# Kernel optimization log

Hardware: AMD Instinct MI355X
Metric: run time of the kernel (lower is better)

Reference implementation:

```python
import jax, jax.numpy as jnp
import numpy as np

B, C, H, W = 16, 512, 32, 32
HW = H * W  # == input_features == output_features for shapes to be consistent


def setup_inputs() -> dict:
    key = jax.random.key(0)
    k1, k2, k3 = jax.random.split(key, 3)
    node1 = jax.random.normal(k1, (B, C, H, W), dtype=jnp.float32)
    node2 = jax.random.normal(k2, (B, C, H, W), dtype=jnp.float32)
    # nn.Linear(input_features, output_features, bias=False).weight: [out, in]
    W_c = jax.random.normal(k3, (HW, HW), dtype=jnp.float32) * (1.0 / np.sqrt(HW))
    return {"node1": node1, "node2": node2, "W_c": W_c}


def reference(node1, node2, W_c):
    b, c, h, w = node1.shape
    hw = h * w
    n1 = node1.reshape(b, c, hw)  # [B, C, HW]
    n2 = node2.reshape(b, c, hw)  # [B, C, HW]
    # x = W_c(n1): Linear applies y = x @ W^T  -> [B, C, HW_out]
    x = jnp.einsum('bch,oh->bco', n1, W_c)
    # e = bmm(x.permute(0,2,1), n2): [B, HW_out, C] @ [B, C, HW] -> [B, HW_out, HW]
    e = jnp.einsum('bco,bch->boh', x, n2)
    a = jax.nn.softmax(e, axis=-1)  # softmax over last dim (HW of node2)
    # m = bmm(n2, a): [B, C, HW] @ [B, HW, HW] -> [B, C, HW]
    m = jnp.einsum('bck,bkj->bcj', n2, a)
    return m
```

## Files before the change

kernel.cpp:

```cpp
#include <hip/hip_runtime.h>
#include <math.h>


typedef _Float16 f16;
typedef _Float16 f16x8 __attribute__((ext_vector_type(8)));
typedef _Float16 f16x4 __attribute__((ext_vector_type(4)));
typedef float f32x4 __attribute__((ext_vector_type(4)));

#define L2E 1.442695040888963f

#define WG_BARRIER() asm volatile("s_waitcnt lgkmcnt(0)\ns_barrier" ::: "memory")

__device__ __forceinline__ f16x8 cvt8(f32x4 lo, f32x4 hi) {
    f16x8 o;
#pragma unroll
    for (int i = 0; i < 4; ++i) { o[i] = (f16)lo[i]; o[4 + i] = (f16)hi[i]; }
    return o;
}

__device__ __forceinline__ f16x8 expb(f16x8 b, f32x4 cl, f32x4 ch) {
    f16x8 t;
#pragma unroll
    for (int i = 0; i < 4; ++i) t[i] = (f16)exp2f(fmaf((float)b[i], L2E, -cl[i]));
#pragma unroll
    for (int i = 0; i < 4; ++i) t[4 + i] = (f16)exp2f(fmaf((float)b[4 + i], L2E, -ch[i]));
    return t;
}

__global__ __launch_bounds__(256) void prep(const float* __restrict__ Wc,
                                            const float* __restrict__ n2,
                                            f16* __restrict__ Wf,
                                            f16* __restrict__ n2t) {
    const int bid = blockIdx.x, tid = threadIdx.x;
    if (bid < 512) {
        const size_t i = ((size_t)bid * 256 + tid) * 8;
        f32x4 a = *(const f32x4*)(Wc + i);
        f32x4 b = *(const f32x4*)(Wc + i + 4);
        *(f16x8*)(Wf + i) = cvt8(a, b);
        return;
    }
    const int id = bid - 512;
    const int b = id >> 7;
    const int ry = (id & 127) >> 4;
    const int cx = id & 15;
    const float* S = n2 + (size_t)b * 512 * 1024;
    f16* Dt = n2t + (size_t)b * 1024 * 512;
    __shared__ f16 Ts[64 * 72];
    const int r0 = ry * 64, c0 = cx * 64;
    const int rr = tid >> 3, cc8 = (tid & 7) * 8;
#pragma unroll
    for (int h = 0; h < 2; ++h) {
        const int row = r0 + rr + 32 * h;
        const float* s = S + (size_t)row * 1024 + c0 + cc8;
        f32x4 a = *(const f32x4*)s, bq = *(const f32x4*)(s + 4);
        *(f16x8*)&Ts[(rr + 32 * h) * 72 + cc8] = cvt8(a, bq);
    }
    __syncthreads();
    const int j = tid >> 2, k16 = (tid & 3) * 16;
    f16* d = Dt + (size_t)(c0 + j) * 512 + r0 + k16;
    f16x8 o0, o1;
#pragma unroll
    for (int i = 0; i < 8; ++i) {
        o0[i] = Ts[(k16 + i) * 72 + j];
        o1[i] = Ts[(k16 + 8 + i) * 72 + j];
    }
    *(f16x8*)d = o0;
    *(f16x8*)(d + 8) = o1;
}

__global__ __launch_bounds__(256) void stats_combine(const float* __restrict__ Pm,
                                                     const float* __restrict__ Ps,
                                                     float* __restrict__ Sc) {
    const int g = blockIdx.x * 256 + threadIdx.x;
    const int b = g >> 10, o = g & 1023;
    const int mt = o >> 8, ml = o & 255;
    const float* pm = Pm + ((size_t)(b * 4 + mt) * 8) * 256 + ml;
    const float* ps = Ps + ((size_t)(b * 4 + mt) * 8) * 256 + ml;
    float M = -3.0e38f;
#pragma unroll
    for (int p = 0; p < 8; ++p) M = fmaxf(M, pm[p * 256]);
    float S = 0.f;
#pragma unroll
    for (int p = 0; p < 8; ++p) S += ps[p * 256] * exp2f(pm[p * 256] - M);
    Sc[g] = M + __log2f(S);
}

template <int NS>
__device__ __forceinline__ void gemm_core(const char* gA0, const char* gA1,
                                          const char* gB, char* SM, int sOff,
                                          int wm, int wn, int col, int swz16,
                                          f32x4 (&acc)[4][4]) {
    f16x8 a00 = *(const f16x8*)gA0, a01 = *(const f16x8*)gA1;
    f16x8 b0 = *(const f16x8*)gB;
    {
        char* dA = SM + sOff;
        *(f16x8*)dA = a00;
        *(f16x8*)(dA + 8192) = a01;
        *(f16x8*)(SM + 32768 + sOff) = b0;
    }
    f16x8 a10 = *(const f16x8*)(gA0 + 64), a11 = *(const f16x8*)(gA1 + 64);
    f16x8 b1 = *(const f16x8*)(gB + 64);
    a00 = *(const f16x8*)(gA0 + 128); a01 = *(const f16x8*)(gA1 + 128);
    b0 = *(const f16x8*)(gB + 128);
    WG_BARRIER();
#pragma unroll
    for (int kb = 0; kb < NS; ++kb) {
        const char* Ac = SM + (kb & 1) * 16384;
        const char* Bc = SM + 32768 + (kb & 1) * 8192;
        f16x8 fa[4], fb[4];
#pragma unroll
        for (int u = 0; u < 4; ++u)
            fa[u] = *(const f16x8*)(Ac + (wm + u * 16 + col) * 64 + swz16);
#pragma unroll
        for (int v = 0; v < 4; ++v)
            fb[v] = *(const f16x8*)(Bc + (wn + v * 16 + col) * 64 + swz16);
#pragma unroll
        for (int u = 0; u < 4; ++u)
#pragma unroll
            for (int v = 0; v < 4; ++v)
                acc[u][v] = __builtin_amdgcn_mfma_f32_16x16x32_f16(fa[u], fb[v],
                                                                   acc[u][v], 0, 0, 0);
        if (kb + 1 < NS) {
            char* dA = SM + ((kb + 1) & 1) * 16384 + sOff;
            char* dB = SM + 32768 + ((kb + 1) & 1) * 8192 + sOff;
            if ((kb & 1) == 0) {
                *(f16x8*)dA = a10;
                *(f16x8*)(dA + 8192) = a11;
                *(f16x8*)dB = b1;
                if (kb + 3 < NS) {
                    a10 = *(const f16x8*)(gA0 + (size_t)(kb + 3) * 64);
                    a11 = *(const f16x8*)(gA1 + (size_t)(kb + 3) * 64);
                    b1 = *(const f16x8*)(gB + (size_t)(kb + 3) * 64);
                }
            } else {
                *(f16x8*)dA = a00;
                *(f16x8*)(dA + 8192) = a01;
                *(f16x8*)dB = b0;
                if (kb + 3 < NS) {
                    a00 = *(const f16x8*)(gA0 + (size_t)(kb + 3) * 64);
                    a01 = *(const f16x8*)(gA1 + (size_t)(kb + 3) * 64);
                    b0 = *(const f16x8*)(gB + (size_t)(kb + 3) * 64);
                }
            }
            WG_BARRIER();
        }
    }
}

template <int NS, bool EXPB>
__device__ __forceinline__ void gemm_core_a32(const char* gA0, const char* gA1,
                                              const char* gB, const float* gSp,
                                              char* SM, int sOff, int wm, int wn,
                                              int col, int swz16, f32x4 (&acc)[4][4]) {
    f32x4 c00, c01, c10, c11;
    f32x4 a00l = *(const f32x4*)gA0, a00h = *(const f32x4*)(gA0 + 16);
    f32x4 a01l = *(const f32x4*)gA1, a01h = *(const f32x4*)(gA1 + 16);
    f16x8 b0 = *(const f16x8*)gB;
    if (EXPB) { c00 = *(const f32x4*)gSp; c01 = *(const f32x4*)(gSp + 4); }
    {
        char* dA = SM + sOff;
        *(f16x8*)dA = cvt8(a00l, a00h);
        *(f16x8*)(dA + 8192) = cvt8(a01l, a01h);
        char* dB = SM + 32768 + sOff;
        *(f16x8*)dB = EXPB ? expb(b0, c00, c01) : b0;
    }
    f32x4 a10l = *(const f32x4*)(gA0 + 128), a10h = *(const f32x4*)(gA0 + 144);
    f32x4 a11l = *(const f32x4*)(gA1 + 128), a11h = *(const f32x4*)(gA1 + 144);
    f16x8 b1 = *(const f16x8*)(gB + 64);
    if (EXPB) { c10 = *(const f32x4*)(gSp + 32); c11 = *(const f32x4*)(gSp + 36); }
    a00l = *(const f32x4*)(gA0 + 256); a00h = *(const f32x4*)(gA0 + 272);
    a01l = *(const f32x4*)(gA1 + 256); a01h = *(const f32x4*)(gA1 + 272);
    b0 = *(const f16x8*)(gB + 128);
    if (EXPB) { c00 = *(const f32x4*)(gSp + 64); c01 = *(const f32x4*)(gSp + 68); }
    WG_BARRIER();
#pragma unroll
    for (int kb = 0; kb < NS; ++kb) {
        const char* Ac = SM + (kb & 1) * 16384;
        const char* Bc = SM + 32768 + (kb & 1) * 8192;
        f16x8 fa[4], fb[4];
#pragma unroll
        for (int u = 0; u < 4; ++u)
            fa[u] = *(const f16x8*)(Ac + (wm + u * 16 + col) * 64 + swz16);
#pragma unroll
        for (int v = 0; v < 4; ++v)
            fb[v] = *(const f16x8*)(Bc + (wn + v * 16 + col) * 64 + swz16);
#pragma unroll
        for (int u = 0; u < 4; ++u)
#pragma unroll
            for (int v = 0; v < 4; ++v)
                acc[u][v] = __builtin_amdgcn_mfma_f32_16x16x32_f16(fa[u], fb[v],
                                                                   acc[u][v], 0, 0, 0);
        if (kb + 1 < NS) {
            char* dA = SM + ((kb + 1) & 1) * 16384 + sOff;
            char* dB = SM + 32768 + ((kb + 1) & 1) * 8192 + sOff;
            if ((kb & 1) == 0) {
                *(f16x8*)dA = cvt8(a10l, a10h);
                *(f16x8*)(dA + 8192) = cvt8(a11l, a11h);
                *(f16x8*)dB = EXPB ? expb(b1, c10, c11) : b1;
                if (kb + 3 < NS) {
                    a10l = *(const f32x4*)(gA0 + (size_t)(kb + 3) * 128);
                    a10h = *(const f32x4*)(gA0 + (size_t)(kb + 3) * 128 + 16);
                    a11l = *(const f32x4*)(gA1 + (size_t)(kb + 3) * 128);
                    a11h = *(const f32x4*)(gA1 + (size_t)(kb + 3) * 128 + 16);
                    b1 = *(const f16x8*)(gB + (size_t)(kb + 3) * 64);
                    if (EXPB) {
                        c10 = *(const f32x4*)(gSp + (size_t)(kb + 3) * 32);
                        c11 = *(const f32x4*)(gSp + (size_t)(kb + 3) * 32 + 4);
                    }
                }
            } else {
                *(f16x8*)dA = cvt8(a00l, a00h);
                *(f16x8*)(dA + 8192) = cvt8(a01l, a01h);
                *(f16x8*)dB = EXPB ? expb(b0, c00, c01) : b0;
                if (kb + 3 < NS) {
                    a00l = *(const f32x4*)(gA0 + (size_t)(kb + 3) * 128);
                    a00h = *(const f32x4*)(gA0 + (size_t)(kb + 3) * 128 + 16);
                    a01l = *(const f32x4*)(gA1 + (size_t)(kb + 3) * 128);
                    a01h = *(const f32x4*)(gA1 + (size_t)(kb + 3) * 128 + 16);
                    b0 = *(const f16x8*)(gB + (size_t)(kb + 3) * 64);
                    if (EXPB) {
                        c00 = *(const f32x4*)(gSp + (size_t)(kb + 3) * 32);
                        c01 = *(const f32x4*)(gSp + (size_t)(kb + 3) * 32 + 4);
                    }
                }
            }
            WG_BARRIER();
        }
    }
}

__device__ __forceinline__ void epilogue_tr(f32x4 (&acc)[4][4], char* SM, f16* dst0,
                                            int dstRow, int m0, int n0, int tid) {
    const int lane = tid & 63, wave = tid >> 6;
    const int col = lane & 15, quad = lane >> 4;
    const int wn = (wave >> 2) * 64;
    const int mh_w = (wave >> 1) & 1;
    const int wm_loc = (wave & 1) * 64;
    const int j = tid >> 2, seg = (tid & 3) * 32;
    WG_BARRIER();
    f16* Tt = (f16*)SM;
#pragma unroll
    for (int mh = 0; mh < 2; ++mh) {
        if (mh_w == mh) {
#pragma unroll
            for (int u = 0; u < 4; ++u)
#pragma unroll
                for (int v = 0; v < 4; ++v) {
                    f16x4 p;
#pragma unroll
                    for (int r = 0; r < 4; ++r) p[r] = (f16)acc[u][v][r];
                    *(f16x4*)&Tt[(wn + v * 16 + col) * 136 + wm_loc + u * 16 + quad * 4] = p;
                }
        }
        WG_BARRIER();
        f16* dst = dst0 + (size_t)(n0 + j) * dstRow + m0 + mh * 128 + seg;
#pragma unroll
        for (int c8 = 0; c8 < 32; c8 += 8)
            *(f16x8*)(dst + c8) = *(const f16x8*)&Tt[j * 136 + seg + c8];
        if (mh == 0) WG_BARRIER();
    }
}

__global__ __launch_bounds__(512) void gemm1_nt_xt(const float* __restrict__ A,
                                                   const f16* __restrict__ Bw,
                                                   f16* __restrict__ Xt) {
    const int K = 1024;
    const int id = blockIdx.x;
    const int xcd = id & 7, loc = id >> 3;
    const int b = xcd * 2 + (loc >> 4);
    const int m0 = ((loc >> 3) & 1) * 256;
    const int n0 = (loc & 7) * 128;
    A += (size_t)b * 512 * K;
    Xt += (size_t)b * 1024 * 512;
    __shared__ __attribute__((aligned(16))) char SM[49152];
    const int tid = threadIdx.x, lane = tid & 63, wave = tid >> 6;
    const int col = lane & 15, quad = lane >> 4;
    const int wm = (wave & 3) * 64, wn = (wave >> 2) * 64;
    const int srow = tid >> 2, sslot = tid & 3;
    const int sOff = srow * 64 + ((sslot ^ ((srow >> 1) & 3)) * 16);
    const int swz16 = (quad ^ ((col >> 1) & 3)) * 16;
    const char* gA0 = (const char*)A + (size_t)(m0 + srow) * K * 4 + sslot * 32;
    const char* gA1 = gA0 + (size_t)128 * K * 4;
    const char* gB = (const char*)Bw + (size_t)(n0 + srow) * K * 2 + sslot * 16;
    f32x4 acc[4][4] = {};
    gemm_core_a32<32, false>(gA0, gA1, gB, nullptr, SM, sOff, wm, wn, col, swz16, acc);
    epilogue_tr(acc, SM, Xt, 512, m0, n0, tid);
}

__global__ __launch_bounds__(512) void gemm2_nt_et(const f16* __restrict__ A,
                                                   const f16* __restrict__ B,
                                                   f16* __restrict__ Et,
                                                   float* __restrict__ Pm,
                                                   float* __restrict__ Ps) {
    const int K = 512;
    const int id = blockIdx.x;
    const int xcd = id & 7, loc = id >> 3;
    const int b = xcd * 2 + (loc >> 5);
    const int m0 = ((loc >> 3) & 3) * 256;
    const int n0 = (loc & 7) * 128;
    A += (size_t)b * 1024 * K;
    B += (size_t)b * 1024 * K;
    Et += (size_t)b * 1024 * 1024;
    __shared__ __attribute__((aligned(16))) char SM[49152];
    const int tid = threadIdx.x, lane = tid & 63, wave = tid >> 6;
    const int col = lane & 15, quad = lane >> 4;
    const int wm = (wave & 3) * 64, wn = (wave >> 2) * 64;
    const int srow = tid >> 2, sslot = tid & 3;
    const int sOff = srow * 64 + ((sslot ^ ((srow >> 1) & 3)) * 16);
    const int swz16 = (quad ^ ((col >> 1) & 3)) * 16;
    const char* gA0 = (const char*)A + (size_t)(m0 + srow) * K * 2 + sslot * 16;
    const char* gA1 = gA0 + (size_t)128 * K * 2;
    const char* gB = (const char*)B + (size_t)(n0 + srow) * K * 2 + sslot * 16;
    f32x4 acc[4][4] = {};
    gemm_core<16>(gA0, gA1, gB, SM, sOff, wm, wn, col, swz16, acc);

    {
        const int wn_e = (wave >> 2) * 64;
        const int mh_w = (wave >> 1) & 1;
        const int wm_loc = (wave & 1) * 64;
        const int j = tid >> 2, seg = (tid & 3) * 32;
        const int scol = tid >> 2, srq = tid & 3;
        WG_BARRIER();
        f16* Tt = (f16*)SM;
#pragma unroll
        for (int mh = 0; mh < 2; ++mh) {
            if (mh_w == mh) {
#pragma unroll
                for (int u = 0; u < 4; ++u)
#pragma unroll
                    for (int v = 0; v < 4; ++v) {
                        f16x4 p;
#pragma unroll
                        for (int r = 0; r < 4; ++r) p[r] = (f16)acc[u][v][r];
                        *(f16x4*)&Tt[(wn_e + v * 16 + col) * 136 + wm_loc + u * 16 + quad * 4] = p;
                    }
            }
            WG_BARRIER();
            f16* dst = Et + (size_t)(n0 + j) * 1024 + m0 + mh * 128 + seg;
#pragma unroll
            for (int c8 = 0; c8 < 32; c8 += 8)
                *(f16x8*)(dst + c8) = *(const f16x8*)&Tt[j * 136 + seg + c8];
            float mx = -3.0e38f;
#pragma unroll
            for (int n = 0; n < 32; ++n) {
                const int row = srq * 32 + ((n + scol) & 31);
                mx = fmaxf(mx, (float)Tt[row * 136 + scol]);
            }
            const float mxl = mx * L2E;
            float s = 0.f;
#pragma unroll
            for (int n = 0; n < 32; ++n) {
                const int row = srq * 32 + ((n + scol) & 31);
                s += exp2f(fmaf((float)Tt[row * 136 + scol], L2E, -mxl));
            }
            float pmv = mxl, psv = s;
#pragma unroll
            for (int d = 1; d < 4; d <<= 1) {
                float om = __shfl_xor(pmv, d, 64);
                float os = __shfl_xor(psv, d, 64);
                float nm = fmaxf(pmv, om);
                psv = psv * exp2f(pmv - nm) + os * exp2f(om - nm);
                pmv = nm;
            }
            if (srq == 0) {
                const int part = (b * 4 + (m0 >> 8)) * 8 + (n0 >> 7);
                const int ml = mh * 128 + scol;
                Pm[(size_t)part * 256 + ml] = pmv;
                Ps[(size_t)part * 256 + ml] = psv;
            }
            if (mh == 0) WG_BARRIER();
        }
    }
}

__global__ __launch_bounds__(512) void gemm3_nt_out(const float* __restrict__ A,
                                                    const f16* __restrict__ Et,
                                                    const float* __restrict__ Sc,
                                                    float* __restrict__ C) {
    const int K = 1024;
    const int id = blockIdx.x;
    const int xcd = id & 7, loc = id >> 3;
    const int b = xcd * 2 + (loc >> 4);
    const int m0 = ((loc >> 3) & 1) * 256;
    const int n0 = (loc & 7) * 128;
    A += (size_t)b * 512 * K;
    Et += (size_t)b * 1024 * K;
    Sc += (size_t)b * 1024;
    C += (size_t)b * 512 * 1024;
    __shared__ __attribute__((aligned(16))) char SM[49152];
    const int tid = threadIdx.x, lane = tid & 63, wave = tid >> 6;
    const int col = lane & 15, quad = lane >> 4;
    const int wm = (wave & 3) * 64, wn = (wave >> 2) * 64;
    const int srow = tid >> 2, sslot = tid & 3;
    const int sOff = srow * 64 + ((sslot ^ ((srow >> 1) & 3)) * 16);
    const int swz16 = (quad ^ ((col >> 1) & 3)) * 16;
    const char* gA0 = (const char*)A + (size_t)(m0 + srow) * K * 4 + sslot * 32;
    const char* gA1 = gA0 + (size_t)128 * K * 4;
    const char* gB = (const char*)Et + (size_t)(n0 + srow) * K * 2 + sslot * 16;
    const float* gSp = Sc + sslot * 8;
    f32x4 acc[4][4] = {};
    gemm_core_a32<32, true>(gA0, gA1, gB, gSp, SM, sOff, wm, wn, col, swz16, acc);

#pragma unroll
    for (int u = 0; u < 4; ++u)
#pragma unroll
        for (int v = 0; v < 4; ++v)
#pragma unroll
            for (int r = 0; r < 4; ++r)
                C[(size_t)(m0 + wm + u * 16 + quad * 4 + r) * 1024 + n0 + wn + v * 16 + col] =
                    acc[u][v][r];
}

extern "C" void kernel_launch(void* const* d_in, const int* in_sizes, int n_in,
                              void* d_out, int out_size, void* d_ws, size_t ws_size,
                              hipStream_t stream) {
    const float* n1 = (const float*)d_in[0];
    const float* n2 = (const float*)d_in[1];
    const float* Wc = (const float*)d_in[2];
    float* out = (float*)d_out;
    char* ws = (char*)d_ws;

    f16* n2t = (f16*)(ws);
    f16* Xt  = (f16*)(ws + (16u << 20));
    f16* Wf  = (f16*)(ws + (32u << 20));
    f16* Et  = (f16*)(ws + (32u << 20));
    float* Pm = (float*)(ws + (64u << 20));
    float* Ps = (float*)(ws + (65u << 20));
    float* Sc = (float*)(ws + (66u << 20));

    prep<<<2560, dim3(256), 0, stream>>>(Wc, n2, Wf, n2t);
    gemm1_nt_xt<<<256, dim3(512), 0, stream>>>(n1, Wf, Xt);
    gemm2_nt_et<<<512, dim3(512), 0, stream>>>(Xt, n2t, Et, Pm, Ps);
    stats_combine<<<64, dim3(256), 0, stream>>>(Pm, Ps, Sc);
    gemm3_nt_out<<<256, dim3(512), 0, stream>>>(n2, Et, Sc, out);
}
```

Before: 204.1 us.

## Use direct global-to-LDS loads in GEMMs and pre-convert node1 to fp16

Replaces the register-staged double-buffered loads in gemm1 and gemm2 with global_load_lds DMA transfers into a swizzled LDS layout, synchronised through vmcnt waits and barriers. To make gemm1 fit this path, node1 is now converted to fp16 in the prep kernel instead of inside gemm1. The aim is to free registers and VALU work spent staging tiles and to overlap global loads with MFMA. The cost is an extra fp16 copy of node1 written to and read back from global memory, plus an added barrier per k-step.

Result: no change. 200.4 us (-1.8%).

```diff
diff --git a/kernel.cpp b/kernel.cpp
--- a/kernel.cpp
+++ b/kernel.cpp
@@ -11,6 +11,11 @@
 
 #define WG_BARRIER() asm volatile("s_waitcnt lgkmcnt(0)\ns_barrier" ::: "memory")
 
+#define DMA16(g, l)                                                             \
+    __builtin_amdgcn_global_load_lds(                                           \
+        (const __attribute__((address_space(1))) void*)(g),                     \
+        (__attribute__((address_space(3))) void*)(l), 16, 0, 0)
+
 __device__ __forceinline__ f16x8 cvt8(f32x4 lo, f32x4 hi) {
     f16x8 o;
 #pragma unroll
@@ -27,19 +32,22 @@
     return t;
 }
 
-__global__ __launch_bounds__(256) void prep(const float* __restrict__ Wc,
+__global__ __launch_bounds__(256) void prep(const float* __restrict__ n1,
+                                            const float* __restrict__ Wc,
                                             const float* __restrict__ n2,
-                                            f16* __restrict__ Wf,
+                                            f16* __restrict__ n1f, f16* __restrict__ Wf,
                                             f16* __restrict__ n2t) {
     const int bid = blockIdx.x, tid = threadIdx.x;
-    if (bid < 512) {
-        const size_t i = ((size_t)bid * 256 + tid) * 8;
-        f32x4 a = *(const f32x4*)(Wc + i);
-        f32x4 b = *(const f32x4*)(Wc + i + 4);
-        *(f16x8*)(Wf + i) = cvt8(a, b);
+    if (bid < 4608) {
+        const float* s = (bid < 4096) ? n1 : Wc;
+        f16* d = (bid < 4096) ? n1f : Wf;
+        const size_t i = ((size_t)(bid < 4096 ? bid : bid - 4096) * 256 + tid) * 8;
+        f32x4 a = *(const f32x4*)(s + i);
+        f32x4 b = *(const f32x4*)(s + i + 4);
+        *(f16x8*)(d + i) = cvt8(a, b);
         return;
     }
-    const int id = bid - 512;
+    const int id = bid - 4608;
     const int b = id >> 7;
     const int ry = (id & 127) >> 4;
     const int cx = id & 15;
@@ -86,25 +94,18 @@
 }
 
 template <int NS>
-__device__ __forceinline__ void gemm_core(const char* gA0, const char* gA1,
-                                          const char* gB, char* SM, int sOff,
-                                          int wm, int wn, int col, int swz16,
-                                          f32x4 (&acc)[4][4]) {
-    f16x8 a00 = *(const f16x8*)gA0, a01 = *(const f16x8*)gA1;
-    f16x8 b0 = *(const f16x8*)gB;
-    {
-        char* dA = SM + sOff;
-        *(f16x8*)dA = a00;
-        *(f16x8*)(dA + 8192) = a01;
-        *(f16x8*)(SM + 32768 + sOff) = b0;
-    }
-    f16x8 a10 = *(const f16x8*)(gA0 + 64), a11 = *(const f16x8*)(gA1 + 64);
-    f16x8 b1 = *(const f16x8*)(gB + 64);
-    a00 = *(const f16x8*)(gA0 + 128); a01 = *(const f16x8*)(gA1 + 128);
-    b0 = *(const f16x8*)(gB + 128);
-    WG_BARRIER();
+__device__ __forceinline__ void gemm_dmac(const char* sA0, const char* sA1,
+                                          const char* sB, char* dA, char* dB,
+                                          char* SM, int wm, int wn, int col,
+                                          int swz16, f32x4 (&acc)[4][4]) {
+    DMA16(sA0, dA); DMA16(sA1, dA + 8192); DMA16(sB, dB);
+    DMA16(sA0 + 64, dA + 16384); DMA16(sA1 + 64, dA + 24576); DMA16(sB + 64, dB + 8192);
 #pragma unroll
     for (int kb = 0; kb < NS; ++kb) {
+        if (kb + 1 < NS) asm volatile("s_waitcnt vmcnt(3)" ::: "memory");
+        else             asm volatile("s_waitcnt vmcnt(0)" ::: "memory");
+        __builtin_amdgcn_s_barrier();
+        asm volatile("" ::: "memory");
         const char* Ac = SM + (kb & 1) * 16384;
         const char* Bc = SM + 32768 + (kb & 1) * 8192;
         f16x8 fa[4], fb[4];
@@ -114,36 +115,21 @@
 #pragma unroll
         for (int v = 0; v < 4; ++v)
             fb[v] = *(const f16x8*)(Bc + (wn + v * 16 + col) * 64 + swz16);
+        asm volatile("s_waitcnt lgkmcnt(0)" ::: "memory");
+        __builtin_amdgcn_s_barrier();
+        asm volatile("" ::: "memory");
+        if (kb + 2 < NS) {
+            const int o = (kb + 2) * 64;
+            char* da = dA + (kb & 1) * 16384;
+            char* db = dB + (kb & 1) * 8192;
+            DMA16(sA0 + o, da); DMA16(sA1 + o, da + 8192); DMA16(sB + o, db);
+        }
 #pragma unroll
         for (int u = 0; u < 4; ++u)
 #pragma unroll
             for (int v = 0; v < 4; ++v)
                 acc[u][v] = __builtin_amdgcn_mfma_f32_16x16x32_f16(fa[u], fb[v],
                                                                    acc[u][v], 0, 0, 0);
-        if (kb + 1 < NS) {
-            char* dA = SM + ((kb + 1) & 1) * 16384 + sOff;
-            char* dB = SM + 32768 + ((kb + 1) & 1) * 8192 + sOff;
-            if ((kb & 1) == 0) {
-                *(f16x8*)dA = a10;
-                *(f16x8*)(dA + 8192) = a11;
-                *(f16x8*)dB = b1;
-                if (kb + 3 < NS) {
-                    a10 = *(const f16x8*)(gA0 + (size_t)(kb + 3) * 64);
-                    a11 = *(const f16x8*)(gA1 + (size_t)(kb + 3) * 64);
-                    b1 = *(const f16x8*)(gB + (size_t)(kb + 3) * 64);
-                }
-            } else {
-                *(f16x8*)dA = a00;
-                *(f16x8*)(dA + 8192) = a01;
-                *(f16x8*)dB = b0;
-                if (kb + 3 < NS) {
-                    a00 = *(const f16x8*)(gA0 + (size_t)(kb + 3) * 64);
-                    a01 = *(const f16x8*)(gA1 + (size_t)(kb + 3) * 64);
-                    b0 = *(const f16x8*)(gB + (size_t)(kb + 3) * 64);
-                }
-            }
-            WG_BARRIER();
-        }
     }
 }
 
@@ -261,29 +247,30 @@
     }
 }
 
-__global__ __launch_bounds__(512) void gemm1_nt_xt(const float* __restrict__ A,
+__global__ __launch_bounds__(512) void gemm1_nt_xt(const f16* __restrict__ A,
                                                    const f16* __restrict__ Bw,
                                                    f16* __restrict__ Xt) {
-    const int K = 1024;
     const int id = blockIdx.x;
     const int xcd = id & 7, loc = id >> 3;
     const int b = xcd * 2 + (loc >> 4);
     const int m0 = ((loc >> 3) & 1) * 256;
     const int n0 = (loc & 7) * 128;
-    A += (size_t)b * 512 * K;
+    A += (size_t)b * 512 * 1024;
     Xt += (size_t)b * 1024 * 512;
     __shared__ __attribute__((aligned(16))) char SM[49152];
     const int tid = threadIdx.x, lane = tid & 63, wave = tid >> 6;
     const int col = lane & 15, quad = lane >> 4;
     const int wm = (wave & 3) * 64, wn = (wave >> 2) * 64;
-    const int srow = tid >> 2, sslot = tid & 3;
-    const int sOff = srow * 64 + ((sslot ^ ((srow >> 1) & 3)) * 16);
     const int swz16 = (quad ^ ((col >> 1) & 3)) * 16;
-    const char* gA0 = (const char*)A + (size_t)(m0 + srow) * K * 4 + sslot * 32;
-    const char* gA1 = gA0 + (size_t)128 * K * 4;
-    const char* gB = (const char*)Bw + (size_t)(n0 + srow) * K * 2 + sslot * 16;
+    const int r = wave * 16 + (lane >> 2), ls = lane & 3;
+    const int x = (r >> 1) & 3;
+    const char* sA0 = (const char*)A + (size_t)(m0 + r) * 2048 + ((ls ^ x) * 16);
+    const char* sA1 = sA0 + (size_t)128 * 2048;
+    const char* sB  = (const char*)Bw + (size_t)(n0 + r) * 2048 + ((ls ^ x) * 16);
+    char* dA = SM + wave * 1024;
+    char* dB = SM + 32768 + wave * 1024;
     f32x4 acc[4][4] = {};
-    gemm_core_a32<32, false>(gA0, gA1, gB, nullptr, SM, sOff, wm, wn, col, swz16, acc);
+    gemm_dmac<32>(sA0, sA1, sB, dA, dB, SM, wm, wn, col, swz16, acc);
     epilogue_tr(acc, SM, Xt, 512, m0, n0, tid);
 }
 
@@ -292,27 +279,28 @@
                                                    f16* __restrict__ Et,
                                                    float* __restrict__ Pm,
                                                    float* __restrict__ Ps) {
-    const int K = 512;
     const int id = blockIdx.x;
     const int xcd = id & 7, loc = id >> 3;
     const int b = xcd * 2 + (loc >> 5);
     const int m0 = ((loc >> 3) & 3) * 256;
     const int n0 = (loc & 7) * 128;
-    A += (size_t)b * 1024 * K;
-    B += (size_t)b * 1024 * K;
+    A += (size_t)b * 1024 * 512;
+    B += (size_t)b * 1024 * 512;
     Et += (size_t)b * 1024 * 1024;
     __shared__ __attribute__((aligned(16))) char SM[49152];
     const int tid = threadIdx.x, lane = tid & 63, wave = tid >> 6;
     const int col = lane & 15, quad = lane >> 4;
     const int wm = (wave & 3) * 64, wn = (wave >> 2) * 64;
-    const int srow = tid >> 2, sslot = tid & 3;
-    const int sOff = srow * 64 + ((sslot ^ ((srow >> 1) & 3)) * 16);
     const int swz16 = (quad ^ ((col >> 1) & 3)) * 16;
-    const char* gA0 = (const char*)A + (size_t)(m0 + srow) * K * 2 + sslot * 16;
-    const char* gA1 = gA0 + (size_t)128 * K * 2;
-    const char* gB = (const char*)B + (size_t)(n0 + srow) * K * 2 + sslot * 16;
+    const int r = wave * 16 + (lane >> 2), ls = lane & 3;
+    const int x = (r >> 1) & 3;
+    const char* sA0 = (const char*)A + (size_t)(m0 + r) * 1024 + ((ls ^ x) * 16);
+    const char* sA1 = sA0 + (size_t)128 * 1024;
+    const char* sB  = (const char*)B + (size_t)(n0 + r) * 1024 + ((ls ^ x) * 16);
+    char* dA = SM + wave * 1024;
+    char* dB = SM + 32768 + wave * 1024;
     f32x4 acc[4][4] = {};
-    gemm_core<16>(gA0, gA1, gB, SM, sOff, wm, wn, col, swz16, acc);
+    gemm_dmac<16>(sA0, sA1, sB, dA, dB, SM, wm, wn, col, swz16, acc);
 
     {
         const int wn_e = (wave >> 2) * 64;
@@ -331,7 +319,7 @@
                     for (int v = 0; v < 4; ++v) {
                         f16x4 p;
 #pragma unroll
-                        for (int r = 0; r < 4; ++r) p[r] = (f16)acc[u][v][r];
+                        for (int r2 = 0; r2 < 4; ++r2) p[r2] = (f16)acc[u][v][r2];
                         *(f16x4*)&Tt[(wn_e + v * 16 + col) * 136 + wm_loc + u * 16 + quad * 4] = p;
                     }
             }
@@ -424,12 +412,13 @@
     f16* Xt  = (f16*)(ws + (16u << 20));
     f16* Wf  = (f16*)(ws + (32u << 20));
     f16* Et  = (f16*)(ws + (32u << 20));
-    float* Pm = (float*)(ws + (64u << 20));
-    float* Ps = (float*)(ws + (65u << 20));
-    float* Sc = (float*)(ws + (66u << 20));
-
-    prep<<<2560, dim3(256), 0, stream>>>(Wc, n2, Wf, n2t);
-    gemm1_nt_xt<<<256, dim3(512), 0, stream>>>(n1, Wf, Xt);
+    f16* n1f = (f16*)(ws + (64u << 20));
+    float* Pm = (float*)(ws + (80u << 20));
+    float* Ps = (float*)(ws + (81u << 20));
+    float* Sc = (float*)(ws + (82u << 20));
+
+    prep<<<6656, dim3(256), 0, stream>>>(n1, Wc, n2, n1f, Wf, n2t);
+    gemm1_nt_xt<<<256, dim3(512), 0, stream>>>(n1f, Wf, Xt);
     gemm2_nt_et<<<512, dim3(512), 0, stream>>>(Xt, n2t, Et, Pm, Ps);
     stats_combine<<<64, dim3(256), 0, stream>>>(Pm, Ps, Sc);
     gemm3_nt_out<<<256, dim3(512), 0, stream>>>(n2, Et, Sc, out);
```
